# Optimization experiments

Measured on AMD Instinct MI355X. Metric: run time of the kernel, lower is better.

Reference implementation:

```python
import jax, jax.numpy as jnp
import numpy as np


def _proj(x_flat, w, b):
    # x_flat: (N, C, L), w: (O, C), b: (O,) -> (N, O, L)  (1x1x1 Conv3d)
    return jnp.einsum('oc,ncl->nol', w, x_flat) + b[None, :, None]


def setup_inputs() -> dict:
    key = jax.random.key(0)
    ks = jax.random.split(key, 9)
    C, Ch = 256, 128
    N, T, H, W = 2, 8, 28, 28
    s_in = 1.0 / np.sqrt(C)
    s_h = 1.0 / np.sqrt(Ch)
    return {
        'x': jax.random.normal(ks[0], (N, C, T, H, W), jnp.float32),
        'g_w': jax.random.normal(ks[1], (Ch, C), jnp.float32) * s_in,
        'g_b': jax.random.normal(ks[2], (Ch,), jnp.float32) * 0.01,
        'theta_w': jax.random.normal(ks[3], (Ch, C), jnp.float32) * s_in,
        'theta_b': jax.random.normal(ks[4], (Ch,), jnp.float32) * 0.01,
        'phi_w': jax.random.normal(ks[5], (Ch, C), jnp.float32) * s_in,
        'phi_b': jax.random.normal(ks[6], (Ch,), jnp.float32) * 0.01,
        'wz_w': jax.random.normal(ks[7], (C, Ch), jnp.float32) * s_h,
        'wz_b': jax.random.normal(ks[8], (C,), jnp.float32) * 0.01,
    }


def reference(x, g_w, g_b, theta_w, theta_b, phi_w, phi_b, wz_w, wz_b):
    N, C, T, H, W = x.shape
    L = T * H * W
    xf = x.reshape(N, C, L)                      # (N, C, L)
    g_x = _proj(xf, g_w, g_b)                    # (N, Ch, L)
    theta_x = _proj(xf, theta_w, theta_b)        # (N, Ch, L)
    phi_x = _proj(xf, phi_w, phi_b)              # (N, Ch, L)
    # f[n, i, j] = theta[n, :, i] . phi[n, :, j]
    f = jnp.einsum('nci,ncj->nij', theta_x, phi_x)  # (N, L, L)
    f = jax.nn.softmax(f, axis=-1)
    # y[n, c, i] = sum_j f[n, i, j] * g[n, c, j]
    y = jnp.einsum('nij,ncj->nci', f, g_x)          # (N, Ch, L)
    z = _proj(y, wz_w, wz_b)                        # (N, C, L)
    return z.reshape(N, C, T, H, W) + x
```

## Files before the change

kernel.cpp:

```cpp
#include <hip/hip_runtime.h>
#include <hip/hip_bf16.h>

constexpr int CIN    = 256;
constexpr int CH     = 128;
constexpr int LSEQ   = 6272;
constexpr int NBATCH = 2;
constexpr int NLCH   = NBATCH * LSEQ * CH;
constexpr float SHIFT = 40.0f;

typedef __attribute__((ext_vector_type(8))) __bf16 bf16x8;
typedef __attribute__((ext_vector_type(4))) float  f32x4;

__device__ __forceinline__ unsigned short f2bf(float f) {
    __hip_bfloat16 h = __float2bfloat16(f);
    return *reinterpret_cast<unsigned short*>(&h);
}
__device__ __forceinline__ float us2f(unsigned short h) {
    return __uint_as_float((unsigned)h << 16);
}

union BF8 { bf16x8 v; unsigned short u[8]; };
union PU  { unsigned u[4]; bf16x8 v; };

__device__ __forceinline__ unsigned cvtpk(float a, float b) {
    unsigned r;
    asm("v_cvt_pk_bf16_f32 %0, %1, %2" : "=v"(r) : "v"(a), "v"(b));
    return r;
}
__device__ __forceinline__ void pl32swap(unsigned &a, unsigned &b) {
    asm("v_permlane32_swap_b32 %0, %1" : "+v"(a), "+v"(b));
}
__device__ __forceinline__ void pl16swap(unsigned &a, unsigned &b) {
    asm("v_permlane16_swap_b32 %0, %1" : "+v"(a), "+v"(b));
}

__device__ __forceinline__ void split8(float4 a, float4 b, bf16x8& hi, bf16x8& lo) {
    BF8 H, L;
    float f[8] = { a.x, a.y, a.z, a.w, b.x, b.y, b.z, b.w };
    #pragma unroll
    for (int p = 0; p < 8; ++p) {
        unsigned short h = f2bf(f[p]);
        H.u[p] = h;
        L.u[p] = f2bf(f[p] - us2f(h));
    }
    hi = H.v; lo = L.v;
}

#define GLDS16(g, l) __builtin_amdgcn_global_load_lds(                      \
    (const __attribute__((address_space(1))) void*)(g),                     \
    (__attribute__((address_space(3))) void*)(l), 16, 0, 0)

__global__ __launch_bounds__(256) void proj_kernel(
    const float* __restrict__ x,
    const float* __restrict__ th_w, const float* __restrict__ th_b,
    const float* __restrict__ ph_w, const float* __restrict__ ph_b,
    const float* __restrict__ gw,   const float* __restrict__ gb,
    unsigned short* __restrict__ q, unsigned short* __restrict__ k,
    unsigned short* __restrict__ vt)
{
    constexpr int XS = 264;
    __shared__ unsigned short xhi[64][XS];
    __shared__ unsigned short xlo[64][XS];
    unsigned short (*gst)[137] = (unsigned short (*)[137])&xhi[0][0];

    const int t    = threadIdx.x;
    const int n    = blockIdx.y;
    const int l0   = blockIdx.x * 64;
    const int w    = t >> 6;
    const int lane = t & 63;
    const int lo   = lane & 15;
    const int quad = lane >> 4;

    {
        const int c = t;
        const float4* xr = (const float4*)(x + (size_t)(n * CIN + c) * LSEQ + l0);
        #pragma unroll
        for (int g4 = 0; g4 < 16; ++g4) {
            float4 v = xr[g4];
            float f[4] = { v.x, v.y, v.z, v.w };
            #pragma unroll
            for (int j = 0; j < 4; ++j) {
                unsigned short h = f2bf(f[j]);
                xhi[g4 * 4 + j][c] = h;
                xlo[g4 * 4 + j][c] = f2bf(f[j] - us2f(h));
            }
        }
    }

    const float* wrp[6]; float biasv[6];
    #pragma unroll
    for (int j = 0; j < 6; ++j) {
        int gch = 96 * w + 16 * j + lo;
        if (gch < 128)      { wrp[j] = th_w + (size_t)gch * CIN;         biasv[j] = th_b[gch]; }
        else if (gch < 256) { wrp[j] = ph_w + (size_t)(gch - 128) * CIN; biasv[j] = ph_b[gch - 128]; }
        else                { wrp[j] = gw   + (size_t)(gch - 256) * CIN; biasv[j] = gb[gch - 256]; }
    }

    f32x4 acc[4][6];
    #pragma unroll
    for (int mt = 0; mt < 4; ++mt)
        #pragma unroll
        for (int j = 0; j < 6; ++j) acc[mt][j] = (f32x4){0.f, 0.f, 0.f, 0.f};

    __syncthreads();

    for (int ks = 0; ks < 8; ++ks) {
        const int k0 = ks * 32 + quad * 8;
        bf16x8 ahi[4], alo[4];
        #pragma unroll
        for (int mt = 0; mt < 4; ++mt) {
            ahi[mt] = *(const bf16x8*)&xhi[mt * 16 + lo][k0];
            alo[mt] = *(const bf16x8*)&xlo[mt * 16 + lo][k0];
        }
        #pragma unroll
        for (int j = 0; j < 6; ++j) {
            const float* p = wrp[j] + k0;
            bf16x8 bhi, blo;
            split8(*(const float4*)p, *(const float4*)(p + 4), bhi, blo);
            #pragma unroll
            for (int mt = 0; mt < 4; ++mt) {
                f32x4 a = acc[mt][j];
                a = __builtin_amdgcn_mfma_f32_16x16x32_bf16(ahi[mt], bhi, a, 0, 0, 0);
                a = __builtin_amdgcn_mfma_f32_16x16x32_bf16(alo[mt], bhi, a, 0, 0, 0);
                a = __builtin_amdgcn_mfma_f32_16x16x32_bf16(ahi[mt], blo, a, 0, 0, 0);
                acc[mt][j] = a;
            }
        }
    }

    __syncthreads();

    #pragma unroll
    for (int j = 0; j < 6; ++j) {
        const int base = 96 * w + 16 * j;
        #pragma unroll
        for (int mt = 0; mt < 4; ++mt) {
            #pragma unroll
            for (int r = 0; r < 4; ++r) {
                float val = acc[mt][j][r] + biasv[j];
                const int lrow = mt * 16 + quad * 4 + r;
                if (base < 256) {
                    unsigned short* dst = (base < 128) ? q : k;
                    const int ch = (base < 128) ? base + lo : base - 128 + lo;
                    dst[(size_t)(n * LSEQ + l0 + lrow) * CH + ch] = f2bf(val);
                } else {
                    gst[lrow][base - 256 + lo] = f2bf(val);
                }
            }
        }
    }
    __syncthreads();

    #pragma unroll
    for (int rep = 0; rep < 16; ++rep) {
        const int flat = rep * 256 + t;
        const int ch   = flat >> 5;
        const int lam  = flat & 31;
        unsigned u = (unsigned)gst[2 * lam][ch] | ((unsigned)gst[2 * lam + 1][ch] << 16);
        ((unsigned*)(vt + (size_t)(n * CH + ch) * LSEQ + l0))[lam] = u;
    }
}

__global__ __launch_bounds__(256, 2) void attn_kernel(
    const unsigned short* __restrict__ qb, const unsigned short* __restrict__ kb,
    const unsigned short* __restrict__ vtg,
    float* __restrict__ Op, float* __restrict__ lp,
    unsigned short* __restrict__ yb, int ns)
{
    constexpr int NTJ = LSEQ / 64;
    __shared__ unsigned short ks [2][64][128];
    __shared__ unsigned short vTs[2][128][64];

    const int t    = threadIdx.x;
    const int s    = blockIdx.y;
    const int n    = blockIdx.z;
    const int i0   = blockIdx.x * 128;
    const int w    = t >> 6;
    const int lane = t & 63;
    const int lo   = lane & 15;
    const int quad = lane >> 4;
    const int lom  = (lo & 7) * 4;

    const int jt0 = (s * NTJ) / ns;
    const int jt1 = ((s + 1) * NTJ) / ns;

    const unsigned short* kbase = kb  + (size_t)n * LSEQ * CH;
    const unsigned short* vbase = vtg + (size_t)n * CH * LSEQ;

    bf16x8 qfrag[2][4];
    #pragma unroll
    for (int nt = 0; nt < 2; ++nt) {
        const unsigned short* qrow =
            qb + (size_t)(n * LSEQ + i0 + 32 * w + nt * 16 + lo) * CH;
        #pragma unroll
        for (int kc = 0; kc < 4; ++kc)
            qfrag[nt][kc] = *(const bf16x8*)(qrow + kc * 32 + quad * 8);
    }

    f32x4 o_acc[2][8];
    #pragma unroll
    for (int mt = 0; mt < 2; ++mt)
        #pragma unroll
        for (int nt = 0; nt < 8; ++nt) o_acc[mt][nt] = (f32x4){0.f, 0.f, 0.f, 0.f};
    float l_r[2] = {0.f, 0.f};

    auto stage = [&](int buf, int jt) {
        const int j0 = jt * 64;
        #pragma unroll
        for (int i = 0; i < 4; ++i) {
            const int c = w * 4 + i;
            {
                const int row = c * 4 + (lane >> 4);
                const int pcol = (lane & 15) * 4;
                const int lcol = pcol ^ ((row & 7) * 4);
                const unsigned short* g = kbase + (size_t)(j0 + row) * CH + lcol * 2;
                GLDS16(g, &ks[buf][0][0] + c * 512);
            }
            {
                const int row = c * 8 + (lane >> 3);
                const int pcol = (lane & 7) * 4;
                const int lcol = pcol ^ ((row & 7) * 4);
                const unsigned short* g = vbase + (size_t)row * LSEQ + j0 + lcol * 2;
                GLDS16(g, &vTs[buf][0][0] + c * 512);
            }
        }
    };

    int buf = 0;
    stage(0, jt0);
    __syncthreads();

    for (int jt = jt0; jt < jt1; ++jt) {
        if (jt + 1 < jt1) stage(buf ^ 1, jt + 1);

        bf16x8 pfrag[2][2];
        #pragma unroll
        for (int kc2 = 0; kc2 < 2; ++kc2) {
            f32x4 sacc[2][2];
            #pragma unroll
            for (int h = 0; h < 2; ++h)
                #pragma unroll
                for (int nt = 0; nt < 2; ++nt) sacc[h][nt] = (f32x4){0.f,0.f,0.f,0.f};
            #pragma unroll
            for (int kc = 0; kc < 4; ++kc) {
                const int pcol = (kc * 16 + quad * 4) ^ lom;
                #pragma unroll
                for (int h = 0; h < 2; ++h) {
                    bf16x8 a = *(const bf16x8*)&ks[buf][(kc2 * 2 + h) * 16 + lo][pcol * 2];
                    #pragma unroll
                    for (int nt = 0; nt < 2; ++nt)
                        sacc[h][nt] = __builtin_amdgcn_mfma_f32_16x16x32_bf16(
                            a, qfrag[nt][kc], sacc[h][nt], 0, 0, 0);
                }
            }
            #pragma unroll
            for (int nt = 0; nt < 2; ++nt) {
                float e[8];
                #pragma unroll
                for (int h = 0; h < 2; ++h)
                    #pragma unroll
                    for (int r = 0; r < 4; ++r) {
                        float p = __expf(sacc[h][nt][r] - SHIFT);
                        l_r[nt] += p;
                        e[h * 4 + r] = p;
                    }
                unsigned A0 = cvtpk(e[0], e[1]);
                unsigned A1 = cvtpk(e[2], e[3]);
                unsigned B0 = cvtpk(e[4], e[5]);
                unsigned B1 = cvtpk(e[6], e[7]);
                pl32swap(A0, B0); pl16swap(A0, B0);
                pl32swap(A1, B1); pl16swap(A1, B1);
                PU pu; pu.u[0] = A0; pu.u[1] = A1; pu.u[2] = B0; pu.u[3] = B1;
                pfrag[nt][kc2] = pu.v;
            }
        }

        #pragma unroll
        for (int nt8 = 0; nt8 < 8; ++nt8) {
            #pragma unroll
            for (int kc = 0; kc < 2; ++kc) {
                const int pcol = (kc * 16 + quad * 4) ^ lom;
                bf16x8 b = *(const bf16x8*)&vTs[buf][nt8 * 16 + lo][pcol * 2];
                #pragma unroll
                for (int mt = 0; mt < 2; ++mt)
                    o_acc[mt][nt8] = __builtin_amdgcn_mfma_f32_16x16x32_bf16(
                        pfrag[mt][kc], b, o_acc[mt][nt8], 0, 0, 0);
            }
        }

        __syncthreads();
        buf ^= 1;
    }

    #pragma unroll
    for (int nt = 0; nt < 2; ++nt) {
        l_r[nt] += __shfl_xor(l_r[nt], 16);
        l_r[nt] += __shfl_xor(l_r[nt], 32);
    }

    if (Op != nullptr) {
        #pragma unroll
        for (int mt = 0; mt < 2; ++mt)
            #pragma unroll
            for (int r = 0; r < 4; ++r) {
                const int qi = i0 + 32 * w + mt * 16 + quad * 4 + r;
                const float lsum = __shfl(l_r[mt], quad * 4 + r);
                float* orow = Op + ((size_t)(n * ns + s) * LSEQ + qi) * CH;
                #pragma unroll
                for (int nt = 0; nt < 8; ++nt)
                    orow[nt * 16 + lo] = o_acc[mt][nt][r];
                if (lo == 0)
                    lp[(size_t)(n * ns + s) * LSEQ + qi] = lsum;
            }
    } else {
        #pragma unroll
        for (int mt = 0; mt < 2; ++mt)
            #pragma unroll
            for (int r = 0; r < 4; ++r) {
                const int qi = i0 + 32 * w + mt * 16 + quad * 4 + r;
                const float lsum = __shfl(l_r[mt], quad * 4 + r);
                const float inv = 1.0f / lsum;
                unsigned short* yr = yb + (size_t)(n * LSEQ + qi) * CH;
                #pragma unroll
                for (int nt = 0; nt < 8; ++nt)
                    yr[nt * 16 + lo] = f2bf(o_acc[mt][nt][r] * inv);
            }
    }
}

__global__ __launch_bounds__(256) void combine_kernel(
    const float* __restrict__ Op, const float* __restrict__ lp,
    unsigned short* __restrict__ yb, int ns)
{
    const int idx = blockIdx.x * 256 + threadIdx.x;
    const int n   = idx / (LSEQ * 32);
    const int rem = idx - n * (LSEQ * 32);
    const int l   = rem >> 5;
    const int c4  = (rem & 31) << 2;

    float4 o = make_float4(0.f, 0.f, 0.f, 0.f);
    float ls = 0.f;
    for (int s = 0; s < ns; ++s) {
        const float4 v = *(const float4*)&Op[((size_t)(n * ns + s) * LSEQ + l) * CH + c4];
        o.x += v.x; o.y += v.y; o.z += v.z; o.w += v.w;
        ls += lp[(size_t)(n * ns + s) * LSEQ + l];
    }
    const float inv = 1.0f / ls;
    unsigned r0 = (unsigned)f2bf(o.x * inv) | ((unsigned)f2bf(o.y * inv) << 16);
    unsigned r1 = (unsigned)f2bf(o.z * inv) | ((unsigned)f2bf(o.w * inv) << 16);
    uint2* dst = (uint2*)(yb + (size_t)(n * LSEQ + l) * CH + c4);
    *dst = make_uint2(r0, r1);
}

__global__ __launch_bounds__(256) void zout_kernel(
    const unsigned short* __restrict__ yb,
    const float* __restrict__ wz_w, const float* __restrict__ wz_b,
    const float* __restrict__ x, float* __restrict__ out)
{
    const int t    = threadIdx.x;
    const int n    = blockIdx.y;
    const int l0   = blockIdx.x * 64;
    const int w    = t >> 6;
    const int lane = t & 63;
    const int lo   = lane & 15;
    const int quad = lane >> 4;

    f32x4 acc[4][4];
    #pragma unroll
    for (int mt = 0; mt < 4; ++mt)
        #pragma unroll
        for (int nt = 0; nt < 4; ++nt) acc[mt][nt] = (f32x4){0.f, 0.f, 0.f, 0.f};

    const unsigned short* yrow[4];
    #pragma unroll
    for (int nt = 0; nt < 4; ++nt)
        yrow[nt] = yb + (size_t)(n * LSEQ + l0 + nt * 16 + lo) * CH;

    #pragma unroll
    for (int ks = 0; ks < 4; ++ks) {
        const int k0 = ks * 32 + quad * 8;
        bf16x8 bfr[4];
        #pragma unroll
        for (int nt = 0; nt < 4; ++nt)
            bfr[nt] = *(const bf16x8*)(yrow[nt] + k0);
        #pragma unroll
        for (int mt = 0; mt < 4; ++mt) {
            const float* p = wz_w + (size_t)(64 * w + mt * 16 + lo) * CH + k0;
            bf16x8 ahi, alo;
            split8(*(const float4*)p, *(const float4*)(p + 4), ahi, alo);
            #pragma unroll
            for (int nt = 0; nt < 4; ++nt) {
                f32x4 a = acc[mt][nt];
                a = __builtin_amdgcn_mfma_f32_16x16x32_bf16(ahi, bfr[nt], a, 0, 0, 0);
                a = __builtin_amdgcn_mfma_f32_16x16x32_bf16(alo, bfr[nt], a, 0, 0, 0);
                acc[mt][nt] = a;
            }
        }
    }

    #pragma unroll
    for (int mt = 0; mt < 4; ++mt) {
        #pragma unroll
        for (int r = 0; r < 4; ++r) {
            const int c = 64 * w + mt * 16 + quad * 4 + r;
            const float bias = wz_b[c];
            const size_t base = (size_t)(n * CIN + c) * LSEQ + l0;
            #pragma unroll
            for (int nt = 0; nt < 4; ++nt) {
                const size_t off = base + nt * 16 + lo;
                out[off] = acc[mt][nt][r] + bias + x[off];
            }
        }
    }
}

extern "C" void kernel_launch(void* const* d_in, const int* in_sizes, int n_in,
                              void* d_out, int out_size, void* d_ws, size_t ws_size,
                              hipStream_t stream) {
    const float* x    = (const float*)d_in[0];
    const float* g_w  = (const float*)d_in[1];
    const float* g_b  = (const float*)d_in[2];
    const float* th_w = (const float*)d_in[3];
    const float* th_b = (const float*)d_in[4];
    const float* ph_w = (const float*)d_in[5];
    const float* ph_b = (const float*)d_in[6];
    const float* wz_w = (const float*)d_in[7];
    const float* wz_b = (const float*)d_in[8];
    float* out = (float*)d_out;

    unsigned short* q  = (unsigned short*)d_ws;
    unsigned short* k  = q + NLCH;
    unsigned short* vt = k + NLCH;
    unsigned short* y  = vt + NLCH;

    const size_t base = (size_t)4 * NLCH * 2;
    const size_t per  = (size_t)NLCH * 4 + (size_t)NBATCH * LSEQ * 4;
    int ns = 0;
    if (ws_size > base) {
        size_t cap = (ws_size - base) / per;
        ns = (cap > 8) ? 8 : (int)cap;
    }

    float* Op = (ns > 0) ? (float*)(y + NLCH) : nullptr;
    float* lp = (ns > 0) ? Op + (size_t)ns * NLCH : nullptr;

    proj_kernel<<<dim3(LSEQ / 64, NBATCH), 256, 0, stream>>>(
        x, th_w, th_b, ph_w, ph_b, g_w, g_b, q, k, vt);

    if (ns > 0) {
        attn_kernel<<<dim3(LSEQ / 128, ns, NBATCH), 256, 0, stream>>>(
            q, k, vt, Op, lp, y, ns);
        combine_kernel<<<(NBATCH * LSEQ * 32) / 256, 256, 0, stream>>>(Op, lp, y, ns);
    } else {
        attn_kernel<<<dim3(LSEQ / 128, 1, NBATCH), 256, 0, stream>>>(
            q, k, vt, nullptr, nullptr, y, 1);
    }

    zout_kernel<<<dim3(LSEQ / 64, NBATCH), 256, 0, stream>>>(y, wz_w, wz_b, x, out);
}
```

Before: 188.9 us.

## Pre-split weights once, fold log2e into Q, fuse split-KV combine into output projection

A new small kernel splits the QKV and Wz weights into bf16 hi/lo pairs once, so the projection kernels no longer redo the float-to-bf16 split in their inner loops. The log2(e) factor is folded into Q during projection, which lets the softmax use the raw v_exp_f32 instruction with a rescaled shift. The separate split-KV combine kernel is removed and its reduction now runs inside zout_kernel, staged through shared memory, which saves one launch and one round trip of y through global memory. In exchange there is an extra weight-prep launch, and Q is rounded to bf16 after scaling.

```diff
diff --git a/kernel.cpp b/kernel.cpp
--- a/kernel.cpp
+++ b/kernel.cpp
@@ -6,7 +6,10 @@
 constexpr int LSEQ   = 6272;
 constexpr int NBATCH = 2;
 constexpr int NLCH   = NBATCH * LSEQ * CH;
-constexpr float SHIFT = 40.0f;
+constexpr int WQKV   = 384 * 256;
+constexpr int WZ     = 256 * 128;
+constexpr float LOG2E  = 1.44269504f;
+constexpr float SHIFT2 = 57.70780163f;
 
 typedef __attribute__((ext_vector_type(8))) __bf16 bf16x8;
 typedef __attribute__((ext_vector_type(4))) float  f32x4;
@@ -33,6 +36,9 @@
 __device__ __forceinline__ void pl16swap(unsigned &a, unsigned &b) {
     asm("v_permlane16_swap_b32 %0, %1" : "+v"(a), "+v"(b));
 }
+__device__ __forceinline__ float vexp2(float x) {
+    float r; asm("v_exp_f32 %0, %1" : "=v"(r) : "v"(x)); return r;
+}
 
 __device__ __forceinline__ void split8(float4 a, float4 b, bf16x8& hi, bf16x8& lo) {
     BF8 H, L;
@@ -50,11 +56,35 @@
     (const __attribute__((address_space(1))) void*)(g),                     \
     (__attribute__((address_space(3))) void*)(l), 16, 0, 0)
 
+__global__ __launch_bounds__(256) void wprep_kernel(
+    const float* __restrict__ th_w, const float* __restrict__ ph_w,
+    const float* __restrict__ gw,   const float* __restrict__ wz_w,
+    unsigned short* __restrict__ wsp, unsigned short* __restrict__ wzsp)
+{
+    const int t = threadIdx.x, b = blockIdx.x;
+    if (b < 48) {
+        const int e   = (b * 256 + t) * 8;
+        const int gch = e >> 8, c = e & 255;
+        const float* src = (gch < 128) ? th_w + ((size_t)gch << 8) + c
+                         : (gch < 256) ? ph_w + ((size_t)(gch - 128) << 8) + c
+                                       : gw   + ((size_t)(gch - 256) << 8) + c;
+        bf16x8 hi, lo;
+        split8(*(const float4*)src, *(const float4*)(src + 4), hi, lo);
+        *(bf16x8*)(wsp + e)        = hi;
+        *(bf16x8*)(wsp + WQKV + e) = lo;
+    } else {
+        const int e = ((b - 48) * 256 + t) * 8;
+        bf16x8 hi, lo;
+        split8(*(const float4*)(wz_w + e), *(const float4*)(wz_w + e + 4), hi, lo);
+        *(bf16x8*)(wzsp + e)      = hi;
+        *(bf16x8*)(wzsp + WZ + e) = lo;
+    }
+}
+
 __global__ __launch_bounds__(256) void proj_kernel(
-    const float* __restrict__ x,
-    const float* __restrict__ th_w, const float* __restrict__ th_b,
-    const float* __restrict__ ph_w, const float* __restrict__ ph_b,
-    const float* __restrict__ gw,   const float* __restrict__ gb,
+    const float* __restrict__ x, const unsigned short* __restrict__ wsp,
+    const float* __restrict__ th_b, const float* __restrict__ ph_b,
+    const float* __restrict__ gb,
     unsigned short* __restrict__ q, unsigned short* __restrict__ k,
     unsigned short* __restrict__ vt)
 {
@@ -87,13 +117,14 @@
         }
     }
 
-    const float* wrp[6]; float biasv[6];
+    const unsigned short* wrp[6]; float biasv[6];
     #pragma unroll
     for (int j = 0; j < 6; ++j) {
         int gch = 96 * w + 16 * j + lo;
-        if (gch < 128)      { wrp[j] = th_w + (size_t)gch * CIN;         biasv[j] = th_b[gch]; }
-        else if (gch < 256) { wrp[j] = ph_w + (size_t)(gch - 128) * CIN; biasv[j] = ph_b[gch - 128]; }
-        else                { wrp[j] = gw   + (size_t)(gch - 256) * CIN; biasv[j] = gb[gch - 256]; }
+        wrp[j] = wsp + (size_t)gch * CIN;
+        if (gch < 128)      biasv[j] = th_b[gch];
+        else if (gch < 256) biasv[j] = ph_b[gch - 128];
+        else                biasv[j] = gb[gch - 256];
     }
 
     f32x4 acc[4][6];
@@ -114,9 +145,9 @@
         }
         #pragma unroll
         for (int j = 0; j < 6; ++j) {
-            const float* p = wrp[j] + k0;
-            bf16x8 bhi, blo;
-            split8(*(const float4*)p, *(const float4*)(p + 4), bhi, blo);
+            const unsigned short* p = wrp[j] + k0;
+            bf16x8 bhi = *(const bf16x8*)p;
+            bf16x8 blo = *(const bf16x8*)(p + WQKV);
             #pragma unroll
             for (int mt = 0; mt < 4; ++mt) {
                 f32x4 a = acc[mt][j];
@@ -142,6 +173,7 @@
                 if (base < 256) {
                     unsigned short* dst = (base < 128) ? q : k;
                     const int ch = (base < 128) ? base + lo : base - 128 + lo;
+                    if (base < 128) val *= LOG2E;
                     dst[(size_t)(n * LSEQ + l0 + lrow) * CH + ch] = f2bf(val);
                 } else {
                     gst[lrow][base - 256 + lo] = f2bf(val);
@@ -260,7 +292,7 @@
                 for (int h = 0; h < 2; ++h)
                     #pragma unroll
                     for (int r = 0; r < 4; ++r) {
-                        float p = __expf(sacc[h][nt][r] - SHIFT);
+                        float p = vexp2(sacc[h][nt][r] - SHIFT2);
                         l_r[nt] += p;
                         e[h * 4 + r] = p;
                     }
@@ -328,35 +360,15 @@
     }
 }
 
-__global__ __launch_bounds__(256) void combine_kernel(
-    const float* __restrict__ Op, const float* __restrict__ lp,
-    unsigned short* __restrict__ yb, int ns)
-{
-    const int idx = blockIdx.x * 256 + threadIdx.x;
-    const int n   = idx / (LSEQ * 32);
-    const int rem = idx - n * (LSEQ * 32);
-    const int l   = rem >> 5;
-    const int c4  = (rem & 31) << 2;
-
-    float4 o = make_float4(0.f, 0.f, 0.f, 0.f);
-    float ls = 0.f;
-    for (int s = 0; s < ns; ++s) {
-        const float4 v = *(const float4*)&Op[((size_t)(n * ns + s) * LSEQ + l) * CH + c4];
-        o.x += v.x; o.y += v.y; o.z += v.z; o.w += v.w;
-        ls += lp[(size_t)(n * ns + s) * LSEQ + l];
-    }
-    const float inv = 1.0f / ls;
-    unsigned r0 = (unsigned)f2bf(o.x * inv) | ((unsigned)f2bf(o.y * inv) << 16);
-    unsigned r1 = (unsigned)f2bf(o.z * inv) | ((unsigned)f2bf(o.w * inv) << 16);
-    uint2* dst = (uint2*)(yb + (size_t)(n * LSEQ + l) * CH + c4);
-    *dst = make_uint2(r0, r1);
-}
-
 __global__ __launch_bounds__(256) void zout_kernel(
     const unsigned short* __restrict__ yb,
-    const float* __restrict__ wz_w, const float* __restrict__ wz_b,
+    const float* __restrict__ Op, const float* __restrict__ lp, int ns,
+    const unsigned short* __restrict__ wzsp, const float* __restrict__ wz_b,
     const float* __restrict__ x, float* __restrict__ out)
 {
+    __shared__ unsigned short ytile[64][136];
+    __shared__ float linv[64];
+
     const int t    = threadIdx.x;
     const int n    = blockIdx.y;
     const int l0   = blockIdx.x * 64;
@@ -365,16 +377,47 @@
     const int lo   = lane & 15;
     const int quad = lane >> 4;
 
+    if (Op != nullptr) {
+        if (t < 64) {
+            float ls = 0.f;
+            for (int sb = 0; sb < ns; ++sb)
+                ls += lp[(size_t)(n * ns + sb) * LSEQ + l0 + t];
+            linv[t] = 1.0f / ls;
+        }
+        __syncthreads();
+        #pragma unroll
+        for (int rep = 0; rep < 8; ++rep) {
+            const int flat4 = rep * 256 + t;
+            const int l  = flat4 >> 5;
+            const int c4 = (flat4 & 31) * 4;
+            float4 o = make_float4(0.f, 0.f, 0.f, 0.f);
+            for (int sb = 0; sb < ns; ++sb) {
+                const float4 v = *(const float4*)
+                    &Op[((size_t)(n * ns + sb) * LSEQ + l0 + l) * CH + c4];
+                o.x += v.x; o.y += v.y; o.z += v.z; o.w += v.w;
+            }
+            const float iv = linv[l];
+            unsigned r0 = (unsigned)f2bf(o.x * iv) | ((unsigned)f2bf(o.y * iv) << 16);
+            unsigned r1 = (unsigned)f2bf(o.z * iv) | ((unsigned)f2bf(o.w * iv) << 16);
+            *(uint2*)&ytile[l][c4] = make_uint2(r0, r1);
+        }
+    } else {
+        #pragma unroll
+        for (int rep = 0; rep < 4; ++rep) {
+            const int flat8 = rep * 256 + t;
+            const int l  = flat8 >> 4;
+            const int c8 = (flat8 & 15) * 8;
+            uint2 v = *(const uint2*)(yb + (size_t)(n * LSEQ + l0 + l) * CH + c8);
+            *(uint2*)&ytile[l][c8] = v;
+        }
+    }
+    __syncthreads();
+
     f32x4 acc[4][4];
     #pragma unroll
     for (int mt = 0; mt < 4; ++mt)
         #pragma unroll
         for (int nt = 0; nt < 4; ++nt) acc[mt][nt] = (f32x4){0.f, 0.f, 0.f, 0.f};
-
-    const unsigned short* yrow[4];
-    #pragma unroll
-    for (int nt = 0; nt < 4; ++nt)
-        yrow[nt] = yb + (size_t)(n * LSEQ + l0 + nt * 16 + lo) * CH;
 
     #pragma unroll
     for (int ks = 0; ks < 4; ++ks) {
@@ -382,12 +425,12 @@
         bf16x8 bfr[4];
         #pragma unroll
         for (int nt = 0; nt < 4; ++nt)
-            bfr[nt] = *(const bf16x8*)(yrow[nt] + k0);
+            bfr[nt] = *(const bf16x8*)&ytile[nt * 16 + lo][k0];
         #pragma unroll
         for (int mt = 0; mt < 4; ++mt) {
-            const float* p = wz_w + (size_t)(64 * w + mt * 16 + lo) * CH + k0;
-            bf16x8 ahi, alo;
-            split8(*(const float4*)p, *(const float4*)(p + 4), ahi, alo);
+            const unsigned short* pa = wzsp + (size_t)(64 * w + mt * 16 + lo) * CH + k0;
+            bf16x8 ahi = *(const bf16x8*)pa;
+            bf16x8 alo = *(const bf16x8*)(pa + WZ);
             #pragma unroll
             for (int nt = 0; nt < 4; ++nt) {
                 f32x4 a = acc[mt][nt];
@@ -428,12 +471,14 @@
     const float* wz_b = (const float*)d_in[8];
     float* out = (float*)d_out;
 
-    unsigned short* q  = (unsigned short*)d_ws;
-    unsigned short* k  = q + NLCH;
-    unsigned short* vt = k + NLCH;
-    unsigned short* y  = vt + NLCH;
-
-    const size_t base = (size_t)4 * NLCH * 2;
+    unsigned short* q    = (unsigned short*)d_ws;
+    unsigned short* k    = q + NLCH;
+    unsigned short* vt   = k + NLCH;
+    unsigned short* y    = vt + NLCH;
+    unsigned short* wsp  = y + NLCH;
+    unsigned short* wzsp = wsp + 2 * WQKV;
+
+    const size_t base = ((size_t)4 * NLCH + 2 * WQKV + 2 * WZ) * 2;
     const size_t per  = (size_t)NLCH * 4 + (size_t)NBATCH * LSEQ * 4;
     int ns = 0;
     if (ws_size > base) {
@@ -441,20 +486,22 @@
         ns = (cap > 8) ? 8 : (int)cap;
     }
 
-    float* Op = (ns > 0) ? (float*)(y + NLCH) : nullptr;
+    float* Op = (ns > 0) ? (float*)(wzsp + 2 * WZ) : nullptr;
     float* lp = (ns > 0) ? Op + (size_t)ns * NLCH : nullptr;
 
+    wprep_kernel<<<64, 256, 0, stream>>>(th_w, ph_w, g_w, wz_w, wsp, wzsp);
+
     proj_kernel<<<dim3(LSEQ / 64, NBATCH), 256, 0, stream>>>(
-        x, th_w, th_b, ph_w, ph_b, g_w, g_b, q, k, vt);
+        x, wsp, th_b, ph_b, g_b, q, k, vt);
 
     if (ns > 0) {
         attn_kernel<<<dim3(LSEQ / 128, ns, NBATCH), 256, 0, stream>>>(
             q, k, vt, Op, lp, y, ns);
-        combine_kernel<<<(NBATCH * LSEQ * 32) / 256, 256, 0, stream>>>(Op, lp, y, ns);
     } else {
         attn_kernel<<<dim3(LSEQ / 128, 1, NBATCH), 256, 0, stream>>>(
             q, k, vt, nullptr, nullptr, y, 1);
     }
 
-    zout_kernel<<<dim3(LSEQ / 64, NBATCH), 256, 0, stream>>>(y, wz_w, wz_b, x, out);
-}
+    zout_kernel<<<dim3(LSEQ / 64, NBATCH), 256, 0, stream>>>(
+        y, Op, lp, ns, wzsp, wz_b, x, out);
+}
```

After: 194.9 us. 3.2% more time.
